# Kernel tuning notes

Measured on AMD Instinct MI355X. Metric: run time of the kernel, lower is better.

Reference implementation:

```python
import jax, jax.numpy as jnp
import numpy as np

N_NODES = 50000
HIDDEN = 512
N_EDGES = 200000
NUM_LAYERS = 2


def setup_inputs() -> dict:
    key = jax.random.key(0)
    ks = jax.random.split(key, 8)
    stdv = 1.0 / np.sqrt(HIDDEN)
    u = lambda k, shape: jax.random.uniform(k, shape, jnp.float32, -stdv, stdv)
    inputs = jnp.arange(N_NODES, dtype=jnp.int64)
    A = jax.random.randint(ks[0], (2, N_EDGES), 0, N_NODES, dtype=jnp.int64)
    emb = u(ks[1], (N_NODES, HIDDEN))            # embedding table
    weight = u(ks[2], (NUM_LAYERS, HIDDEN, HIDDEN))  # per-layer edge transform
    w_ih = u(ks[3], (3 * HIDDEN, HIDDEN))        # GRUCell input weights (r,z,n)
    w_hh = u(ks[4], (3 * HIDDEN, HIDDEN))        # GRUCell hidden weights
    b_ih = u(ks[5], (3 * HIDDEN,))
    b_hh = u(ks[6], (3 * HIDDEN,))
    return {"inputs": inputs, "A": A, "emb": emb, "weight": weight,
            "w_ih": w_ih, "w_hh": w_hh, "b_ih": b_ih, "b_hh": b_hh}


def _gru_cell(m, h, w_ih, w_hh, b_ih, b_hh):
    # torch.nn.GRUCell math, gate order (r, z, n)
    gi = m @ w_ih.T + b_ih
    gh = h @ w_hh.T + b_hh
    i_r, i_z, i_n = jnp.split(gi, 3, axis=-1)
    h_r, h_z, h_n = jnp.split(gh, 3, axis=-1)
    r = jax.nn.sigmoid(i_r + h_r)
    z = jax.nn.sigmoid(i_z + h_z)
    n = jnp.tanh(i_n + r * h_n)
    return (1.0 - z) * n + z * h


def reference(inputs, A, emb, weight, w_ih, w_hh, b_ih, b_hh):
    x = emb[inputs]                      # [N, C] embedding gather
    src, dst = A[0], A[1]
    n = x.shape[0]
    for l in range(NUM_LAYERS):
        m = x @ weight[l]                # [N, C] per-layer transform
        agg = jax.ops.segment_sum(m[src], dst, num_segments=n)  # scatter-add messages
        x = _gru_cell(agg, x, w_ih, w_hh, b_ih, b_hh)
    return x
```

## Files before the change

### kernel.cpp

```cpp
#include <hip/hip_runtime.h>
#include <stdint.h>

#define N_NODES 50000
#define HIDDEN  512
#define N_EDGES 200000

#define BK 32
#define LDP 40

typedef __attribute__((ext_vector_type(8))) short   short8;
typedef __attribute__((ext_vector_type(4))) float   floatx4;

__device__ inline float bf2f(ushort u) {
    union { uint32_t u; float f; } v; v.u = ((uint32_t)u) << 16; return v.f;
}
__device__ inline ushort f2bf(float f) {
    union { float f; uint32_t u; } v; v.f = f;
    uint32_t r = v.u + 0x7fffu + ((v.u >> 16) & 1u);
    return (ushort)(r >> 16);
}
__device__ inline floatx4 mfma16(short8 a, short8 b, floatx4 c) {
    return __builtin_amdgcn_mfma_f32_16x16x32_bf16(a, b, c, 0, 0, 0);
}
__device__ inline bool idx_is64(const int* __restrict__ inputs) {
    return inputs[1] == 0 && inputs[2] == 1;
}

__global__ void k_gather(const int* __restrict__ inputs, const float* __restrict__ emb,
                         ushort* __restrict__ xb) {
    bool is64 = idx_is64(inputs);
    int t = blockIdx.x * blockDim.x + threadIdx.x;
    int row = t >> 6, s8 = (t & 63) << 3;
    if (row >= N_NODES) return;
    int srow = is64 ? inputs[2 * row] : inputs[row];
    srow = srow < 0 ? 0 : (srow >= N_NODES ? N_NODES - 1 : srow);
    const float* src = emb + (size_t)srow * HIDDEN + s8;
    float4 v0 = *(const float4*)(src);
    float4 v1 = *(const float4*)(src + 4);
    ushort o[8] = { f2bf(v0.x), f2bf(v0.y), f2bf(v0.z), f2bf(v0.w),
                    f2bf(v1.x), f2bf(v1.y), f2bf(v1.z), f2bf(v1.w) };
    *(uint4*)(xb + (size_t)row * HIDDEN + s8) = *(uint4*)o;
}

__global__ void k_cvt8(const float* __restrict__ src, ushort* __restrict__ dst, int n) {
    int t = blockIdx.x * blockDim.x + threadIdx.x;
    int base = t * 8;
    if (base >= n) return;
    float4 v0 = *(const float4*)(src + base);
    float4 v1 = *(const float4*)(src + base + 4);
    ushort o[8] = { f2bf(v0.x), f2bf(v0.y), f2bf(v0.z), f2bf(v0.w),
                    f2bf(v1.x), f2bf(v1.y), f2bf(v1.z), f2bf(v1.w) };
    *(uint4*)(dst + base) = *(uint4*)o;
}

__global__ __launch_bounds__(256) void k_gemm_w(const ushort* __restrict__ Aw,
                                                const ushort* __restrict__ Bw,
                                                ushort* __restrict__ Cw) {
    __shared__ ushort As[128][LDP];
    __shared__ ushort Bs[128][LDP];
    const int l = blockIdx.z;
    const ushort* Bp = Bw + (size_t)l * HIDDEN * HIDDEN;
    ushort* Cp = Cw + (size_t)l * 3 * HIDDEN * HIDDEN;
    const int n0 = blockIdx.x * 128, c0 = blockIdx.y * 128;
    const int t = threadIdx.x;
    const int wave = t >> 6, lane = t & 63;
    const int wm = (wave >> 1) << 6, wn = (wave & 1) << 6;
    const int fr = lane & 15, fk = (lane >> 4) << 3;
    const int lm = t >> 2, lk = (t & 3) << 3;
    floatx4 acc[4][4] = {};

    for (int k0 = 0; k0 < HIDDEN; k0 += BK) {
        *(uint4*)&As[lm][lk]      = *(const uint4*)(Aw + (size_t)(n0 + lm) * HIDDEN + k0 + lk);
        *(uint4*)&As[64 + lm][lk] = *(const uint4*)(Aw + (size_t)(n0 + 64 + lm) * HIDDEN + k0 + lk);
        *(uint4*)&Bs[lm][lk]      = *(const uint4*)(Bp + (size_t)(c0 + lm) * HIDDEN + k0 + lk);
        *(uint4*)&Bs[64 + lm][lk] = *(const uint4*)(Bp + (size_t)(c0 + 64 + lm) * HIDDEN + k0 + lk);
        __syncthreads();
        short8 aa[4], bb[4];
        #pragma unroll
        for (int i = 0; i < 4; ++i) {
            aa[i] = *(const short8*)&As[wm + i * 16 + fr][fk];
            bb[i] = *(const short8*)&Bs[wn + i * 16 + fr][fk];
        }
        #pragma unroll
        for (int i = 0; i < 4; ++i)
            #pragma unroll
            for (int j = 0; j < 4; ++j)
                acc[i][j] = mfma16(aa[i], bb[j], acc[i][j]);
        __syncthreads();
    }
    const int er = (lane >> 4) << 2, ec = lane & 15;
    #pragma unroll
    for (int i = 0; i < 4; ++i)
        #pragma unroll
        for (int j = 0; j < 4; ++j)
            #pragma unroll
            for (int r = 0; r < 4; ++r) {
                int row = n0 + wm + i * 16 + er + r;
                Cp[(size_t)row * HIDDEN + c0 + wn + j * 16 + ec] = f2bf(acc[i][j][r]);
            }
}

__global__ void k_hist(const int* __restrict__ inputs, const int* __restrict__ A,
                       int* __restrict__ count) {
    bool is64 = idx_is64(inputs);
    int e = blockIdx.x * blockDim.x + threadIdx.x;
    if (e >= N_EDGES) return;
    int d = is64 ? A[2 * (N_EDGES + e)] : A[N_EDGES + e];
    if (d < 0 || d >= N_NODES) return;
    atomicAdd(count + d, 1);
}

#define SCAN_T 1024
__global__ __launch_bounds__(SCAN_T) void k_scan(const int* __restrict__ count,
                                                 int* __restrict__ row_start,
                                                 int* __restrict__ cursor) {
    __shared__ int part[SCAN_T];
    const int t = threadIdx.x;
    const int chunk = (N_NODES + SCAN_T - 1) / SCAN_T;
    const int base = t * chunk;
    int s = 0;
    for (int i = 0; i < chunk; ++i) {
        int idx = base + i;
        if (idx < N_NODES) s += count[idx];
    }
    part[t] = s;
    __syncthreads();
    for (int off = 1; off < SCAN_T; off <<= 1) {
        int add = (t >= off) ? part[t - off] : 0;
        __syncthreads();
        part[t] += add;
        __syncthreads();
    }
    int running = (t == 0) ? 0 : part[t - 1];
    for (int i = 0; i < chunk; ++i) {
        int idx = base + i;
        if (idx < N_NODES) {
            row_start[idx] = running;
            cursor[idx] = running;
            running += count[idx];
        }
    }
    if (t == 0) row_start[N_NODES] = part[SCAN_T - 1];
}

__global__ void k_place(const int* __restrict__ inputs, const int* __restrict__ A,
                        int* __restrict__ cursor, int* __restrict__ esrc) {
    bool is64 = idx_is64(inputs);
    int e = blockIdx.x * blockDim.x + threadIdx.x;
    if (e >= N_EDGES) return;
    int s, d;
    if (is64) { s = A[2 * e]; d = A[2 * (N_EDGES + e)]; }
    else      { s = A[e];     d = A[N_EDGES + e]; }
    if (s < 0 || s >= N_NODES || d < 0 || d >= N_NODES) return;
    int pos = atomicAdd(cursor + d, 1);
    esrc[pos] = s;
}

__global__ __launch_bounds__(256) void k_agg(const int* __restrict__ row_start,
                                             const int* __restrict__ esrc,
                                             const ushort* __restrict__ x,
                                             ushort* __restrict__ ax) {
    int node = blockIdx.x * 4 + (threadIdx.x >> 6);
    if (node >= N_NODES) return;
    int lane = threadIdx.x & 63;
    int q = lane << 3;
    int beg = row_start[node], end = row_start[node + 1];
    float acc[8] = {};
    for (int i = beg; i < end; ++i) {
        int s = esrc[i];
        uint4 v = *(const uint4*)(x + (size_t)s * HIDDEN + q);
        const ushort* u = (const ushort*)&v;
        #pragma unroll
        for (int j = 0; j < 8; ++j) acc[j] += bf2f(u[j]);
    }
    ushort o[8];
    #pragma unroll
    for (int j = 0; j < 8; ++j) o[j] = f2bf(acc[j]);
    *(uint4*)(ax + (size_t)node * HIDDEN + q) = *(uint4*)o;
}

template<bool F32OUT>
__global__ __launch_bounds__(256) void k_gru(const ushort* __restrict__ agg,
                                             const ushort* __restrict__ xb_cur,
                                             const ushort* __restrict__ wih,
                                             const ushort* __restrict__ whh,
                                             const float* __restrict__ b_ih,
                                             const float* __restrict__ b_hh,
                                             ushort* __restrict__ outB,
                                             float* __restrict__ outF) {
    __shared__ ushort Ag[64][LDP];
    __shared__ ushort Xs[64][LDP];
    __shared__ ushort Wsh[6][64][LDP];
    const int n0 = blockIdx.x * 64, c0 = blockIdx.y * 64;
    const int t = threadIdx.x;
    const int wave = t >> 6, lane = t & 63;
    const int wm = (wave >> 1) << 5, wn = (wave & 1) << 5;
    const int fr = lane & 15, fk = (lane >> 4) << 3;
    const int lm = t >> 2, lk = (t & 3) << 3;
    floatx4 a_sr[2][2] = {}, a_sz[2][2] = {}, a_in[2][2] = {}, a_hn[2][2] = {};

    for (int k0 = 0; k0 < HIDDEN; k0 += BK) {
        int gr = n0 + lm;
        uint4 av = {0, 0, 0, 0}, xv = {0, 0, 0, 0};
        if (gr < N_NODES) {
            av = *(const uint4*)(agg    + (size_t)gr * HIDDEN + k0 + lk);
            xv = *(const uint4*)(xb_cur + (size_t)gr * HIDDEN + k0 + lk);
        }
        *(uint4*)&Ag[lm][lk] = av;
        *(uint4*)&Xs[lm][lk] = xv;
        #pragma unroll
        for (int g = 0; g < 3; ++g) {
            *(uint4*)&Wsh[g][lm][lk] =
                *(const uint4*)(wih + (size_t)(g * HIDDEN + c0 + lm) * HIDDEN + k0 + lk);
            *(uint4*)&Wsh[3 + g][lm][lk] =
                *(const uint4*)(whh + (size_t)(g * HIDDEN + c0 + lm) * HIDDEN + k0 + lk);
        }
        __syncthreads();
        short8 aa[2], ax[2];
        #pragma unroll
        for (int i = 0; i < 2; ++i) {
            aa[i] = *(const short8*)&Ag[wm + i * 16 + fr][fk];
            ax[i] = *(const short8*)&Xs[wm + i * 16 + fr][fk];
        }
        #define GATE(g, A, ACC) { \
            short8 b0 = *(const short8*)&Wsh[g][wn + fr][fk]; \
            short8 b1 = *(const short8*)&Wsh[g][wn + 16 + fr][fk]; \
            _Pragma("unroll") \
            for (int i = 0; i < 2; ++i) { \
                ACC[i][0] = mfma16(A[i], b0, ACC[i][0]); \
                ACC[i][1] = mfma16(A[i], b1, ACC[i][1]); } }
        GATE(0, aa, a_sr)
        GATE(3, ax, a_sr)
        GATE(1, aa, a_sz)
        GATE(4, ax, a_sz)
        GATE(2, aa, a_in)
        GATE(5, ax, a_hn)
        #undef GATE
        __syncthreads();
    }
    const int er = (lane >> 4) << 2, ec = lane & 15;
    #pragma unroll
    for (int j = 0; j < 2; ++j) {
        int col = c0 + wn + j * 16 + ec;
        float bir = b_ih[col] + b_hh[col];
        float biz = b_ih[HIDDEN + col] + b_hh[HIDDEN + col];
        float bin = b_ih[2 * HIDDEN + col];
        float bhn = b_hh[2 * HIDDEN + col];
        #pragma unroll
        for (int i = 0; i < 2; ++i)
            #pragma unroll
            for (int r = 0; r < 4; ++r) {
                int row = n0 + wm + i * 16 + er + r;
                if (row >= N_NODES) continue;
                float vsr = a_sr[i][j][r] + bir;
                float vsz = a_sz[i][j][r] + biz;
                float vin = a_in[i][j][r] + bin;
                float vhn = a_hn[i][j][r] + bhn;
                float rr = 1.f / (1.f + __expf(-vsr));
                float zz = 1.f / (1.f + __expf(-vsz));
                float nn = tanhf(vin + rr * vhn);
                float h  = bf2f(xb_cur[(size_t)row * HIDDEN + col]);
                float out = (1.f - zz) * nn + zz * h;
                if (F32OUT) outF[(size_t)row * HIDDEN + col] = out;
                else        outB[(size_t)row * HIDDEN + col] = f2bf(out);
            }
    }
}

extern "C" void kernel_launch(void* const* d_in, const int* in_sizes, int n_in,
                              void* d_out, int out_size, void* d_ws, size_t ws_size,
                              hipStream_t stream) {
    const int*   inputs = (const int*)d_in[0];
    const int*   A      = (const int*)d_in[1];
    const float* emb    = (const float*)d_in[2];
    const float* weight = (const float*)d_in[3];
    const float* w_ih   = (const float*)d_in[4];
    const float* w_hh   = (const float*)d_in[5];
    const float* b_ih   = (const float*)d_in[6];
    const float* b_hh   = (const float*)d_in[7];

    char* ws = (char*)d_ws;
    size_t off = 0;
    auto alloc = [&](size_t bytes) { void* p = ws + off; off += (bytes + 255) & ~255ull; return p; };
    ushort* WihB      = (ushort*)alloc((size_t)3 * HIDDEN * HIDDEN * sizeof(ushort));
    ushort* WhhB      = (ushort*)alloc((size_t)3 * HIDDEN * HIDDEN * sizeof(ushort));
    ushort* Wb        = (ushort*)alloc((size_t)2 * HIDDEN * HIDDEN * sizeof(ushort));
    ushort* Wc        = (ushort*)alloc((size_t)2 * 3 * HIDDEN * HIDDEN * sizeof(ushort));
    ushort* bufA      = (ushort*)alloc((size_t)N_NODES * HIDDEN * sizeof(ushort));
    ushort* bufB      = (ushort*)alloc((size_t)N_NODES * HIDDEN * sizeof(ushort));
    int*    count     = (int*)alloc((size_t)N_NODES * sizeof(int));
    int*    row_start = (int*)alloc((size_t)(N_NODES + 1) * sizeof(int));
    int*    cursor    = (int*)alloc((size_t)N_NODES * sizeof(int));
    int*    esrc      = (int*)alloc((size_t)N_EDGES * sizeof(int));
    ushort* ax0       = (ushort*)d_out;

    const int nW3 = 3 * HIDDEN * HIDDEN, nW2 = 2 * HIDDEN * HIDDEN;
    k_cvt8<<<(nW3 / 8 + 255) / 256, 256, 0, stream>>>(w_ih, WihB, nW3);
    k_cvt8<<<(nW3 / 8 + 255) / 256, 256, 0, stream>>>(w_hh, WhhB, nW3);
    k_cvt8<<<(nW2 / 8 + 255) / 256, 256, 0, stream>>>(weight, Wb, nW2);
    k_gemm_w<<<dim3(12, 4, 2), 256, 0, stream>>>(WihB, Wb, Wc);

    k_gather<<<(N_NODES * 64 + 255) / 256, 256, 0, stream>>>(inputs, emb, bufA);

    hipMemsetAsync(count, 0, (size_t)N_NODES * sizeof(int), stream);
    k_hist<<<(N_EDGES + 255) / 256, 256, 0, stream>>>(inputs, A, count);
    k_scan<<<1, SCAN_T, 0, stream>>>(count, row_start, cursor);
    k_place<<<(N_EDGES + 255) / 256, 256, 0, stream>>>(inputs, A, cursor, esrc);

    dim3 gGru((N_NODES + 63) / 64, HIDDEN / 64);
    dim3 ga((N_NODES + 3) / 4);

    k_agg<<<ga, 256, 0, stream>>>(row_start, esrc, bufA, ax0);
    k_gru<false><<<gGru, 256, 0, stream>>>(ax0, bufA, Wc, WhhB, b_ih, b_hh, bufB, nullptr);

    k_agg<<<ga, 256, 0, stream>>>(row_start, esrc, bufB, bufA);
    k_gru<true><<<gGru, 256, 0, stream>>>(bufA, bufB, Wc + (size_t)3 * HIDDEN * HIDDEN,
                                          WhhB, b_ih, b_hh, nullptr, (float*)d_out);
}
```

Before: 1.000 ms.

## Rewrite GRU GEMM with 32x32 MFMA, pre-packed fragment weights and LDS-direct loads

Weights for the fused GRU GEMM are pre-packed into an MFMA-fragment layout so each wave loads its B operands straight from global memory into registers, prefetching the next k-slice. Activations are staged into LDS with global_load_lds, and the kernel switches to 32x32x16 MFMA with 128-row tiles and a 1D grid ordered so column blocks of the same row tile run together. The goal is to cut LDS traffic and synchronisation per k-step and raise MFMA efficiency. In exchange it holds more accumulator registers per wave and relies on weights being reused from cache.

Measured after the change: 1.224 ms. 22.4% more time.

```diff
diff --git a/kernel.cpp b/kernel.cpp
--- a/kernel.cpp
+++ b/kernel.cpp
@@ -7,9 +7,11 @@
 
 #define BK 32
 #define LDP 40
-
-typedef __attribute__((ext_vector_type(8))) short   short8;
-typedef __attribute__((ext_vector_type(4))) float   floatx4;
+#define NBX ((N_NODES + 127) / 128)
+
+typedef __attribute__((ext_vector_type(8)))  short short8;
+typedef __attribute__((ext_vector_type(4)))  float floatx4;
+typedef __attribute__((ext_vector_type(16))) float floatx16;
 
 __device__ inline float bf2f(ushort u) {
     union { uint32_t u; float f; } v; v.u = ((uint32_t)u) << 16; return v.f;
@@ -21,6 +23,14 @@
 }
 __device__ inline floatx4 mfma16(short8 a, short8 b, floatx4 c) {
     return __builtin_amdgcn_mfma_f32_16x16x32_bf16(a, b, c, 0, 0, 0);
+}
+__device__ inline floatx16 mfma32(short8 a, short8 b, floatx16 c) {
+    return __builtin_amdgcn_mfma_f32_32x32x16_bf16(a, b, c, 0, 0, 0);
+}
+__device__ inline void gld16(const void* g, void* l) {
+    __builtin_amdgcn_global_load_lds(
+        (const __attribute__((address_space(1))) unsigned int*)g,
+        (__attribute__((address_space(3))) unsigned int*)l, 16, 0, 0);
 }
 __device__ inline bool idx_is64(const int* __restrict__ inputs) {
     return inputs[1] == 0 && inputs[2] == 1;
@@ -51,6 +61,13 @@
     ushort o[8] = { f2bf(v0.x), f2bf(v0.y), f2bf(v0.z), f2bf(v0.w),
                     f2bf(v1.x), f2bf(v1.y), f2bf(v1.z), f2bf(v1.w) };
     *(uint4*)(dst + base) = *(uint4*)o;
+}
+
+__device__ inline size_t wf_index(int grow, int k) {
+    int g3 = grow >> 9, gcol = grow & 511;
+    int cb = gcol >> 5, llo = gcol & 31;
+    int kk = k >> 4, hi = (k >> 3) & 1, jj = k & 7;
+    return ((((size_t)g3 * 16 + cb) * 32 + kk) * 64 + llo + hi * 32) * 8 + jj;
 }
 
 __global__ __launch_bounds__(256) void k_gemm_w(const ushort* __restrict__ Aw,
@@ -95,9 +112,21 @@
         for (int j = 0; j < 4; ++j)
             #pragma unroll
             for (int r = 0; r < 4; ++r) {
-                int row = n0 + wm + i * 16 + er + r;
-                Cp[(size_t)row * HIDDEN + c0 + wn + j * 16 + ec] = f2bf(acc[i][j][r]);
+                int grow = n0 + wm + i * 16 + er + r;
+                int kcol = c0 + wn + j * 16 + ec;
+                Cp[wf_index(grow, kcol)] = f2bf(acc[i][j][r]);
             }
+}
+
+__global__ void k_pack_hh(const float* __restrict__ whh, ushort* __restrict__ wfh) {
+    int t = blockIdx.x * blockDim.x + threadIdx.x;
+    if (t >= 3 * HIDDEN * HIDDEN / 8) return;
+    int grow = t >> 6, k = (t & 63) << 3;
+    const float* src = whh + (size_t)grow * HIDDEN + k;
+    ushort o[8];
+    #pragma unroll
+    for (int j = 0; j < 8; ++j) o[j] = f2bf(src[j]);
+    *(uint4*)(wfh + wf_index(grow, k)) = *(uint4*)o;
 }
 
 __global__ void k_hist(const int* __restrict__ inputs, const int* __restrict__ A,
@@ -180,90 +209,103 @@
 }
 
 template<bool F32OUT>
-__global__ __launch_bounds__(256) void k_gru(const ushort* __restrict__ agg,
-                                             const ushort* __restrict__ xb_cur,
-                                             const ushort* __restrict__ wih,
-                                             const ushort* __restrict__ whh,
-                                             const float* __restrict__ b_ih,
-                                             const float* __restrict__ b_hh,
-                                             ushort* __restrict__ outB,
-                                             float* __restrict__ outF) {
-    __shared__ ushort Ag[64][LDP];
-    __shared__ ushort Xs[64][LDP];
-    __shared__ ushort Wsh[6][64][LDP];
-    const int n0 = blockIdx.x * 64, c0 = blockIdx.y * 64;
-    const int t = threadIdx.x;
-    const int wave = t >> 6, lane = t & 63;
-    const int wm = (wave >> 1) << 5, wn = (wave & 1) << 5;
-    const int fr = lane & 15, fk = (lane >> 4) << 3;
-    const int lm = t >> 2, lk = (t & 3) << 3;
-    floatx4 a_sr[2][2] = {}, a_sz[2][2] = {}, a_in[2][2] = {}, a_hn[2][2] = {};
-
-    for (int k0 = 0; k0 < HIDDEN; k0 += BK) {
-        int gr = n0 + lm;
-        uint4 av = {0, 0, 0, 0}, xv = {0, 0, 0, 0};
-        if (gr < N_NODES) {
-            av = *(const uint4*)(agg    + (size_t)gr * HIDDEN + k0 + lk);
-            xv = *(const uint4*)(xb_cur + (size_t)gr * HIDDEN + k0 + lk);
-        }
-        *(uint4*)&Ag[lm][lk] = av;
-        *(uint4*)&Xs[lm][lk] = xv;
-        #pragma unroll
-        for (int g = 0; g < 3; ++g) {
-            *(uint4*)&Wsh[g][lm][lk] =
-                *(const uint4*)(wih + (size_t)(g * HIDDEN + c0 + lm) * HIDDEN + k0 + lk);
-            *(uint4*)&Wsh[3 + g][lm][lk] =
-                *(const uint4*)(whh + (size_t)(g * HIDDEN + c0 + lm) * HIDDEN + k0 + lk);
-        }
-        __syncthreads();
-        short8 aa[2], ax[2];
-        #pragma unroll
-        for (int i = 0; i < 2; ++i) {
-            aa[i] = *(const short8*)&Ag[wm + i * 16 + fr][fk];
-            ax[i] = *(const short8*)&Xs[wm + i * 16 + fr][fk];
-        }
-        #define GATE(g, A, ACC) { \
-            short8 b0 = *(const short8*)&Wsh[g][wn + fr][fk]; \
-            short8 b1 = *(const short8*)&Wsh[g][wn + 16 + fr][fk]; \
-            _Pragma("unroll") \
-            for (int i = 0; i < 2; ++i) { \
-                ACC[i][0] = mfma16(A[i], b0, ACC[i][0]); \
-                ACC[i][1] = mfma16(A[i], b1, ACC[i][1]); } }
-        GATE(0, aa, a_sr)
-        GATE(3, ax, a_sr)
-        GATE(1, aa, a_sz)
-        GATE(4, ax, a_sz)
-        GATE(2, aa, a_in)
-        GATE(5, ax, a_hn)
-        #undef GATE
-        __syncthreads();
-    }
-    const int er = (lane >> 4) << 2, ec = lane & 15;
+__global__ __launch_bounds__(256, 2) void k_gru2(
+    const ushort* __restrict__ agg, const ushort* __restrict__ xb_cur,
+    const ushort* __restrict__ wfc,
+    const ushort* __restrict__ wfh,
+    const float* __restrict__ b_ih, const float* __restrict__ b_hh,
+    ushort* __restrict__ outB, float* __restrict__ outF)
+{
+    __shared__ ushort Ag[8 * 128 * 8];
+    __shared__ ushort Xs[8 * 128 * 8];
+    const int bid = blockIdx.x;
+    const int by = bid & 7, bx = bid >> 3;
+    const int n0 = bx * 128;
+    const int t = threadIdx.x, w = t >> 6, lane = t & 63;
+    const int wrow = (w >> 1) << 6;
+    const int cb = (by << 1) + (w & 1);
+    const int lrow = lane & 31, lhi = lane >> 5;
+
+    floatx16 a_sr[2] = {}, a_sz[2] = {}, a_in[2] = {}, a_hn[2] = {};
+
+    const ushort* wB0 = wfc;
+    const ushort* wB1 = wfc + 262144;
+    const ushort* wB2 = wfc + 524288;
+    const ushort* wB3 = wfh;
+    const ushort* wB4 = wfh + 262144;
+    const ushort* wB5 = wfh + 524288;
+
+    for (int k0 = 0; k0 < HIDDEN; k0 += 64) {
+        #pragma unroll
+        for (int q = 0; q < 4; ++q) {
+            const int ci = (w * 4 + q) * 64 + lane;
+            const int kh = ci >> 7, row = ci & 127;
+            int gr = n0 + row; if (gr >= N_NODES) gr = N_NODES - 1;
+            const size_t go = (size_t)gr * HIDDEN + k0 + kh * 8;
+            gld16(agg + go,    (void*)((char*)Ag + (size_t)(w * 4 + q) * 1024));
+            gld16(xb_cur + go, (void*)((char*)Xs + (size_t)(w * 4 + q) * 1024));
+        }
+        const int kk0 = k0 >> 4;
+        const size_t fb = ((size_t)cb * 32 + kk0) * 512 + (size_t)lane * 8;
+        short8 b0 = *(const short8*)(wB0 + fb);
+        short8 b1 = *(const short8*)(wB1 + fb);
+        short8 b2 = *(const short8*)(wB2 + fb);
+        short8 b3 = *(const short8*)(wB3 + fb);
+        short8 b4 = *(const short8*)(wB4 + fb);
+        short8 b5 = *(const short8*)(wB5 + fb);
+        __syncthreads();
+        #pragma unroll
+        for (int s = 0; s < 4; ++s) {
+            short8 p0, p1, p2, p3, p4, p5;
+            if (s < 3) {
+                const size_t fn = fb + (size_t)(s + 1) * 512;
+                p0 = *(const short8*)(wB0 + fn);
+                p1 = *(const short8*)(wB1 + fn);
+                p2 = *(const short8*)(wB2 + fn);
+                p3 = *(const short8*)(wB3 + fn);
+                p4 = *(const short8*)(wB4 + fn);
+                p5 = *(const short8*)(wB5 + fn);
+            }
+            const int khl = 2 * s + lhi;
+            #pragma unroll
+            for (int rf = 0; rf < 2; ++rf) {
+                const int row = wrow + rf * 32 + lrow;
+                short8 av = *(const short8*)(Ag + ((size_t)khl * 128 + row) * 8);
+                short8 xv = *(const short8*)(Xs + ((size_t)khl * 128 + row) * 8);
+                a_sr[rf] = mfma32(av, b0, a_sr[rf]);
+                a_sr[rf] = mfma32(xv, b3, a_sr[rf]);
+                a_sz[rf] = mfma32(av, b1, a_sz[rf]);
+                a_sz[rf] = mfma32(xv, b4, a_sz[rf]);
+                a_in[rf] = mfma32(av, b2, a_in[rf]);
+                a_hn[rf] = mfma32(xv, b5, a_hn[rf]);
+            }
+            if (s < 3) { b0 = p0; b1 = p1; b2 = p2; b3 = p3; b4 = p4; b5 = p5; }
+        }
+        __syncthreads();
+    }
+    const int colL = (cb << 5) + lrow;
+    const float bir = b_ih[colL] + b_hh[colL];
+    const float biz = b_ih[HIDDEN + colL] + b_hh[HIDDEN + colL];
+    const float bin = b_ih[2 * HIDDEN + colL];
+    const float bhn = b_hh[2 * HIDDEN + colL];
     #pragma unroll
-    for (int j = 0; j < 2; ++j) {
-        int col = c0 + wn + j * 16 + ec;
-        float bir = b_ih[col] + b_hh[col];
-        float biz = b_ih[HIDDEN + col] + b_hh[HIDDEN + col];
-        float bin = b_ih[2 * HIDDEN + col];
-        float bhn = b_hh[2 * HIDDEN + col];
-        #pragma unroll
-        for (int i = 0; i < 2; ++i)
-            #pragma unroll
-            for (int r = 0; r < 4; ++r) {
-                int row = n0 + wm + i * 16 + er + r;
-                if (row >= N_NODES) continue;
-                float vsr = a_sr[i][j][r] + bir;
-                float vsz = a_sz[i][j][r] + biz;
-                float vin = a_in[i][j][r] + bin;
-                float vhn = a_hn[i][j][r] + bhn;
-                float rr = 1.f / (1.f + __expf(-vsr));
-                float zz = 1.f / (1.f + __expf(-vsz));
-                float nn = tanhf(vin + rr * vhn);
-                float h  = bf2f(xb_cur[(size_t)row * HIDDEN + col]);
-                float out = (1.f - zz) * nn + zz * h;
-                if (F32OUT) outF[(size_t)row * HIDDEN + col] = out;
-                else        outB[(size_t)row * HIDDEN + col] = f2bf(out);
-            }
+    for (int rf = 0; rf < 2; ++rf) {
+        #pragma unroll
+        for (int rg = 0; rg < 16; ++rg) {
+            const int row = n0 + wrow + rf * 32 + (rg & 3) + ((rg >> 2) << 3) + (lhi << 2);
+            if (row >= N_NODES) continue;
+            float vsr = a_sr[rf][rg] + bir;
+            float vsz = a_sz[rf][rg] + biz;
+            float vin = a_in[rf][rg] + bin;
+            float vhn = a_hn[rf][rg] + bhn;
+            float rr = 1.f / (1.f + __expf(-vsr));
+            float zz = 1.f / (1.f + __expf(-vsz));
+            float nn = tanhf(vin + rr * vhn);
+            float h  = bf2f(xb_cur[(size_t)row * HIDDEN + colL]);
+            float out = (1.f - zz) * nn + zz * h;
+            if (F32OUT) outF[(size_t)row * HIDDEN + colL] = out;
+            else        outB[(size_t)row * HIDDEN + colL] = f2bf(out);
+        }
     }
 }
 
@@ -283,9 +325,9 @@
     size_t off = 0;
     auto alloc = [&](size_t bytes) { void* p = ws + off; off += (bytes + 255) & ~255ull; return p; };
     ushort* WihB      = (ushort*)alloc((size_t)3 * HIDDEN * HIDDEN * sizeof(ushort));
-    ushort* WhhB      = (ushort*)alloc((size_t)3 * HIDDEN * HIDDEN * sizeof(ushort));
     ushort* Wb        = (ushort*)alloc((size_t)2 * HIDDEN * HIDDEN * sizeof(ushort));
-    ushort* Wc        = (ushort*)alloc((size_t)2 * 3 * HIDDEN * HIDDEN * sizeof(ushort));
+    ushort* WFc       = (ushort*)alloc((size_t)2 * 3 * HIDDEN * HIDDEN * sizeof(ushort));
+    ushort* WFhh      = (ushort*)alloc((size_t)3 * HIDDEN * HIDDEN * sizeof(ushort));
     ushort* bufA      = (ushort*)alloc((size_t)N_NODES * HIDDEN * sizeof(ushort));
     ushort* bufB      = (ushort*)alloc((size_t)N_NODES * HIDDEN * sizeof(ushort));
     int*    count     = (int*)alloc((size_t)N_NODES * sizeof(int));
@@ -295,10 +337,12 @@
     ushort* ax0       = (ushort*)d_out;
 
     const int nW3 = 3 * HIDDEN * HIDDEN, nW2 = 2 * HIDDEN * HIDDEN;
+    const size_t WF_L = (size_t)3 * HIDDEN * HIDDEN;
+
     k_cvt8<<<(nW3 / 8 + 255) / 256, 256, 0, stream>>>(w_ih, WihB, nW3);
-    k_cvt8<<<(nW3 / 8 + 255) / 256, 256, 0, stream>>>(w_hh, WhhB, nW3);
     k_cvt8<<<(nW2 / 8 + 255) / 256, 256, 0, stream>>>(weight, Wb, nW2);
-    k_gemm_w<<<dim3(12, 4, 2), 256, 0, stream>>>(WihB, Wb, Wc);
+    k_pack_hh<<<(nW3 / 8 + 255) / 256, 256, 0, stream>>>(w_hh, WFhh);
+    k_gemm_w<<<dim3(12, 4, 2), 256, 0, stream>>>(WihB, Wb, WFc);
 
     k_gather<<<(N_NODES * 64 + 255) / 256, 256, 0, stream>>>(inputs, emb, bufA);
 
@@ -307,13 +351,13 @@
     k_scan<<<1, SCAN_T, 0, stream>>>(count, row_start, cursor);
     k_place<<<(N_EDGES + 255) / 256, 256, 0, stream>>>(inputs, A, cursor, esrc);
 
-    dim3 gGru((N_NODES + 63) / 64, HIDDEN / 64);
+    dim3 gGru(NBX * 8);
     dim3 ga((N_NODES + 3) / 4);
 
     k_agg<<<ga, 256, 0, stream>>>(row_start, esrc, bufA, ax0);
-    k_gru<false><<<gGru, 256, 0, stream>>>(ax0, bufA, Wc, WhhB, b_ih, b_hh, bufB, nullptr);
+    k_gru2<false><<<gGru, 256, 0, stream>>>(ax0, bufA, WFc, WFhh, b_ih, b_hh, bufB, nullptr);
 
     k_agg<<<ga, 256, 0, stream>>>(row_start, esrc, bufB, bufA);
-    k_gru<true><<<gGru, 256, 0, stream>>>(bufA, bufB, Wc + (size_t)3 * HIDDEN * HIDDEN,
-                                          WhhB, b_ih, b_hh, nullptr, (float*)d_out);
-}
+    k_gru2<true><<<gGru, 256, 0, stream>>>(bufA, bufB, WFc + WF_L, WFhh, b_ih, b_hh,
+                                           nullptr, (float*)d_out);
+}
```
